# Kernel tuning notes

Measured on AMD Instinct MI355X. Metric: run time of the kernel, lower is better.

The kernel has to match this reference:

```python
import jax, jax.numpy as jnp
import numpy as np

B, F, C, H, W = 2, 128, 3, 720, 1280
NF = 1  # num_filters


def setup_inputs() -> dict:
    key = jax.random.key(0)
    k1, k2, k3, _ = jax.random.split(key, 4)
    f = jax.random.normal(k1, (B, F, H, W), jnp.float32)
    x = jax.random.normal(k2, (B, C, H, W), jnp.float32)
    Wc = jax.random.normal(k3, (NF * 9, F), jnp.float32) * 0.05  # 1x1 conv weight
    bc = jnp.zeros((NF * 9,), jnp.float32)  # bias filled with 0 per module init
    return {"f": f, "x": x, "Wc": Wc, "bc": bc}


def _filter3x3(k, x):
    # k: [B, 9, H, W] per-pixel normalized 3x3 kernels; x: [B, C, H, W]
    b, c, h, w = x.shape
    xp = jnp.pad(x, ((0, 0), (0, 0), (1, 1), (1, 1)))
    # 9 shifted neighborhood views -> [B, 9, C, H, W]
    patches = jnp.stack(
        [xp[:, :, dy:dy + h, dx:dx + w] for dy in range(3) for dx in range(3)],
        axis=1,
    )
    # per-pixel weighted combine of 3x3 neighborhood
    return jnp.einsum('bihw,bichw->bchw', k, patches)


def reference(f, x, Wc, bc):
    # 1x1 conv (quantize=False path): [B,F,H,W] x [9,F] -> [B,9,H,W]
    logits = jnp.einsum('bfhw,of->bohw', f, Wc) + bc[None, :, None, None]
    # softmax over the 9 kernel taps (channel dim), num_filters=1
    k = jax.nn.softmax(logits, axis=1)
    return _filter3x3(k, x)
```

## Files before the change

kernel.cpp:

```cpp
#include <hip/hip_runtime.h>


#define BB 2
#define FF 128
#define CC 3
#define HH 720
#define WW 1280
#define PPT 4
#define BLOCK 256

__global__ __launch_bounds__(BLOCK) void filter3x3_kernel(
    const float* __restrict__ f,
    const float* __restrict__ x,
    const float* __restrict__ Wc,
    const float* __restrict__ bc,
    float* __restrict__ out)
{
    __shared__ float sW[9][FF];
    __shared__ float sb[9];

    const int tid = threadIdx.x;
    for (int i = tid; i < 9 * FF; i += BLOCK) sW[i / FF][i % FF] = Wc[i];
    if (tid < 9) sb[tid] = bc[tid];
    __syncthreads();

    const int t   = blockIdx.x * BLOCK + tid;
    const int WG  = WW / PPT;
    const int w4  = t % WG;
    const int tmp = t / WG;
    const int h   = tmp % HH;
    const int b   = tmp / HH;
    const int w   = w4 * PPT;

    float acc[9][PPT];
    #pragma unroll
    for (int o = 0; o < 9; ++o) {
        const float bv = sb[o];
        #pragma unroll
        for (int p = 0; p < PPT; ++p) acc[o][p] = bv;
    }

    const size_t planeF = (size_t)HH * WW;
    const float* fp = f + ((size_t)b * FF * HH + h) * WW + w;

    #pragma unroll 4
    for (int ch = 0; ch < FF; ++ch) {
        const float4 fv = *(const float4*)(fp + (size_t)ch * planeF);
        #pragma unroll
        for (int o = 0; o < 9; ++o) {
            const float wv = sW[o][ch];
            acc[o][0] = fmaf(fv.x, wv, acc[o][0]);
            acc[o][1] = fmaf(fv.y, wv, acc[o][1]);
            acc[o][2] = fmaf(fv.z, wv, acc[o][2]);
            acc[o][3] = fmaf(fv.w, wv, acc[o][3]);
        }
    }

    #pragma unroll
    for (int p = 0; p < PPT; ++p) {
        float m = acc[0][p];
        #pragma unroll
        for (int o = 1; o < 9; ++o) m = fmaxf(m, acc[o][p]);
        float s = 0.f;
        #pragma unroll
        for (int o = 0; o < 9; ++o) {
            const float e = __expf(acc[o][p] - m);
            acc[o][p] = e;
            s += e;
        }
        const float inv = 1.f / s;
        #pragma unroll
        for (int o = 0; o < 9; ++o) acc[o][p] *= inv;
    }

    #pragma unroll
    for (int c = 0; c < CC; ++c) {
        float o0 = 0.f, o1 = 0.f, o2 = 0.f, o3 = 0.f;
        #pragma unroll
        for (int dy = 0; dy < 3; ++dy) {
            const int row = h + dy - 1;
            const bool vr = (row >= 0) && (row < HH);
            const float* xr = x + ((size_t)(b * CC + c) * HH + row) * WW;
            float xv[PPT + 2];
            #pragma unroll
            for (int j = 0; j < PPT + 2; ++j) {
                const int col = w - 1 + j;
                xv[j] = (vr && col >= 0 && col < WW) ? xr[col] : 0.f;
            }
            #pragma unroll
            for (int dx = 0; dx < 3; ++dx) {
                const int o = dy * 3 + dx;
                o0 = fmaf(acc[o][0], xv[dx + 0], o0);
                o1 = fmaf(acc[o][1], xv[dx + 1], o1);
                o2 = fmaf(acc[o][2], xv[dx + 2], o2);
                o3 = fmaf(acc[o][3], xv[dx + 3], o3);
            }
        }
        float4 ov = make_float4(o0, o1, o2, o3);
        *(float4*)(out + ((size_t)(b * CC + c) * HH + h) * WW + w) = ov;
    }
}

extern "C" void kernel_launch(void* const* d_in, const int* in_sizes, int n_in,
                              void* d_out, int out_size, void* d_ws, size_t ws_size,
                              hipStream_t stream) {
    const float* f  = (const float*)d_in[0];
    const float* x  = (const float*)d_in[1];
    const float* Wc = (const float*)d_in[2];
    const float* bc = (const float*)d_in[3];
    float* out = (float*)d_out;

    const int total_threads = BB * HH * (WW / PPT);
    const int grid = total_threads / BLOCK;
    filter3x3_kernel<<<grid, BLOCK, 0, stream>>>(f, x, Wc, bc, out);
}
```

Baseline: 1.194 ms.

## Software-pipeline feature loads with register prefetch buffer and vectorize weight reads

Adds an explicit 8-deep register prefetch of float4 feature-channel loads, so memory latency for the next channels overlaps the FMAs on the current ones. Weights are transposed in shared memory to [ch][12], so each channel's 9 weights come from two float4 reads and one scalar. An interior fast path skips the bounds checks in the 3x3 filter stage. The prefetch costs extra registers, which may lower occupancy in this memory-bound kernel.

```diff
diff --git a/kernel.cpp b/kernel.cpp
--- a/kernel.cpp
+++ b/kernel.cpp
@@ -8,6 +8,7 @@
 #define WW 1280
 #define PPT 4
 #define BLOCK 256
+#define PIPE 8
 
 __global__ __launch_bounds__(BLOCK) void filter3x3_kernel(
     const float* __restrict__ f,
@@ -16,12 +17,14 @@
     const float* __restrict__ bc,
     float* __restrict__ out)
 {
-    __shared__ float sW[9][FF];
-    __shared__ float sb[9];
+    __shared__ float sW[FF][12];
 
     const int tid = threadIdx.x;
-    for (int i = tid; i < 9 * FF; i += BLOCK) sW[i / FF][i % FF] = Wc[i];
-    if (tid < 9) sb[tid] = bc[tid];
+    for (int i = tid; i < 9 * FF; i += BLOCK) {
+        const int o  = i / FF;
+        const int ch = i % FF;
+        sW[ch][o] = Wc[i];
+    }
     __syncthreads();
 
     const int t   = blockIdx.x * BLOCK + tid;
@@ -35,7 +38,7 @@
     float acc[9][PPT];
     #pragma unroll
     for (int o = 0; o < 9; ++o) {
-        const float bv = sb[o];
+        const float bv = bc[o];
         #pragma unroll
         for (int p = 0; p < PPT; ++p) acc[o][p] = bv;
     }
@@ -43,17 +46,39 @@
     const size_t planeF = (size_t)HH * WW;
     const float* fp = f + ((size_t)b * FF * HH + h) * WW + w;
 
-    #pragma unroll 4
-    for (int ch = 0; ch < FF; ++ch) {
-        const float4 fv = *(const float4*)(fp + (size_t)ch * planeF);
+    float4 buf[PIPE];
+    #pragma unroll
+    for (int j = 0; j < PIPE; ++j)
+        buf[j] = *(const float4*)(fp + (size_t)j * planeF);
+
+    #define FMA_CH(ch_, fv_)                                                 \
+    {                                                                        \
+        const float4 wa = *(const float4*)&sW[(ch_)][0];                     \
+        const float4 wb = *(const float4*)&sW[(ch_)][4];                     \
+        const float  w8 = sW[(ch_)][8];                                      \
+        const float wv[9] = {wa.x, wa.y, wa.z, wa.w, wb.x, wb.y, wb.z, wb.w, w8}; \
+        _Pragma("unroll")                                                    \
+        for (int o = 0; o < 9; ++o) {                                        \
+            acc[o][0] = fmaf((fv_).x, wv[o], acc[o][0]);                     \
+            acc[o][1] = fmaf((fv_).y, wv[o], acc[o][1]);                     \
+            acc[o][2] = fmaf((fv_).z, wv[o], acc[o][2]);                     \
+            acc[o][3] = fmaf((fv_).w, wv[o], acc[o][3]);                     \
+        }                                                                    \
+    }
+
+    #pragma unroll 1
+    for (int c0 = 0; c0 < FF - PIPE; c0 += PIPE) {
         #pragma unroll
-        for (int o = 0; o < 9; ++o) {
-            const float wv = sW[o][ch];
-            acc[o][0] = fmaf(fv.x, wv, acc[o][0]);
-            acc[o][1] = fmaf(fv.y, wv, acc[o][1]);
-            acc[o][2] = fmaf(fv.z, wv, acc[o][2]);
-            acc[o][3] = fmaf(fv.w, wv, acc[o][3]);
+        for (int j = 0; j < PIPE; ++j) {
+            const float4 fv = buf[j];
+            buf[j] = *(const float4*)(fp + (size_t)(c0 + j + PIPE) * planeF);
+            FMA_CH(c0 + j, fv);
         }
+    }
+    #pragma unroll
+    for (int j = 0; j < PIPE; ++j) {
+        const float4 fv = buf[j];
+        FMA_CH(FF - PIPE + j, fv);
     }
 
     #pragma unroll
@@ -73,32 +98,58 @@
         for (int o = 0; o < 9; ++o) acc[o][p] *= inv;
     }
 
-    #pragma unroll
-    for (int c = 0; c < CC; ++c) {
-        float o0 = 0.f, o1 = 0.f, o2 = 0.f, o3 = 0.f;
+    const bool interior = (h >= 1) & (h < HH - 1) & (w >= 4) & (w <= WW - 8);
+    if (interior) {
         #pragma unroll
-        for (int dy = 0; dy < 3; ++dy) {
-            const int row = h + dy - 1;
-            const bool vr = (row >= 0) && (row < HH);
-            const float* xr = x + ((size_t)(b * CC + c) * HH + row) * WW;
-            float xv[PPT + 2];
+        for (int c = 0; c < CC; ++c) {
+            float o0 = 0.f, o1 = 0.f, o2 = 0.f, o3 = 0.f;
             #pragma unroll
-            for (int j = 0; j < PPT + 2; ++j) {
-                const int col = w - 1 + j;
-                xv[j] = (vr && col >= 0 && col < WW) ? xr[col] : 0.f;
+            for (int dy = 0; dy < 3; ++dy) {
+                const float* xr = x + ((size_t)(b * CC + c) * HH + (h + dy - 1)) * WW + w;
+                float xv[PPT + 2];
+                #pragma unroll
+                for (int j = 0; j < PPT + 2; ++j) xv[j] = xr[j - 1];
+                #pragma unroll
+                for (int dx = 0; dx < 3; ++dx) {
+                    const int o = dy * 3 + dx;
+                    o0 = fmaf(acc[o][0], xv[dx + 0], o0);
+                    o1 = fmaf(acc[o][1], xv[dx + 1], o1);
+                    o2 = fmaf(acc[o][2], xv[dx + 2], o2);
+                    o3 = fmaf(acc[o][3], xv[dx + 3], o3);
+                }
             }
+            *(float4*)(out + ((size_t)(b * CC + c) * HH + h) * WW + w) =
+                make_float4(o0, o1, o2, o3);
+        }
+    } else {
+        #pragma unroll
+        for (int c = 0; c < CC; ++c) {
+            float o0 = 0.f, o1 = 0.f, o2 = 0.f, o3 = 0.f;
             #pragma unroll
-            for (int dx = 0; dx < 3; ++dx) {
-                const int o = dy * 3 + dx;
-                o0 = fmaf(acc[o][0], xv[dx + 0], o0);
-                o1 = fmaf(acc[o][1], xv[dx + 1], o1);
-                o2 = fmaf(acc[o][2], xv[dx + 2], o2);
-                o3 = fmaf(acc[o][3], xv[dx + 3], o3);
+            for (int dy = 0; dy < 3; ++dy) {
+                const int row = h + dy - 1;
+                const bool vr = (row >= 0) && (row < HH);
+                const float* xr = x + ((size_t)(b * CC + c) * HH + row) * WW;
+                float xv[PPT + 2];
+                #pragma unroll
+                for (int j = 0; j < PPT + 2; ++j) {
+                    const int col = w - 1 + j;
+                    xv[j] = (vr && col >= 0 && col < WW) ? xr[col] : 0.f;
+                }
+                #pragma unroll
+                for (int dx = 0; dx < 3; ++dx) {
+                    const int o = dy * 3 + dx;
+                    o0 = fmaf(acc[o][0], xv[dx + 0], o0);
+                    o1 = fmaf(acc[o][1], xv[dx + 1], o1);
+                    o2 = fmaf(acc[o][2], xv[dx + 2], o2);
+                    o3 = fmaf(acc[o][3], xv[dx + 3], o3);
+                }
             }
+            *(float4*)(out + ((size_t)(b * CC + c) * HH + h) * WW + w) =
+                make_float4(o0, o1, o2, o3);
         }
-        float4 ov = make_float4(o0, o1, o2, o3);
-        *(float4*)(out + ((size_t)(b * CC + c) * HH + h) * WW + w) = ov;
     }
+    #undef FMA_CH
 }
 
 extern "C" void kernel_launch(void* const* d_in, const int* in_sizes, int n_in,
```

Result: no change. 1.208 ms (+1.2%).
